# Performance work log

Hardware: AMD Instinct MI355X
Metric: run time of the kernel (lower is better)

## Reference

```python
import jax, jax.numpy as jnp
import numpy as np

N, NS, C, S = 262144, 8, 32, 8  # points, nsample, out_channels, share_channels
EPS = 1e-5

def _bn(x, g, b, axes):
    m = jnp.mean(x, axis=axes, keepdims=True)
    v = jnp.mean((x - m) ** 2, axis=axes, keepdims=True)
    return g * (x - m) * jax.lax.rsqrt(v + EPS) + b

def setup_inputs() -> dict:
    key = jax.random.key(0)
    ks = jax.random.split(key, 16)
    lin = lambda k, i, o: (jax.random.normal(k, (o, i), jnp.float32) / np.sqrt(i)).astype(jnp.float32)
    return {
        'p': jax.random.normal(ks[0], (N, 3), jnp.float32) * 10.0,
        'x': jax.random.normal(ks[1], (N, C), jnp.float32),
        'idx': jax.random.randint(ks[2], (N, NS), 0, N, jnp.int32),
        'Wq': lin(ks[3], C, C), 'bq': jnp.zeros((C,), jnp.float32),
        'Wk': lin(ks[4], C, C), 'bk': jnp.zeros((C,), jnp.float32),
        'Wv': lin(ks[5], C, C), 'bv': jnp.zeros((C,), jnp.float32),
        'Wp1': lin(ks[6], 3, 3), 'bp1': jnp.zeros((3,), jnp.float32),
        'gp': jnp.ones((3,), jnp.float32), 'bp': jnp.zeros((3,), jnp.float32),
        'Wp2': lin(ks[7], 3, C), 'bp2': jnp.zeros((C,), jnp.float32),
        'gw1': jnp.ones((C,), jnp.float32), 'bw1': jnp.zeros((C,), jnp.float32),
        'Ww1': lin(ks[8], C, C // S), 'bww1': jnp.zeros((C // S,), jnp.float32),
        'gw2': jnp.ones((C // S,), jnp.float32), 'bw2': jnp.zeros((C // S,), jnp.float32),
        'Ww2': lin(ks[9], C // S, C // S), 'bww2': jnp.zeros((C // S,), jnp.float32),
    }

def reference(p, x, idx, Wq, bq, Wk, bk, Wv, bv, Wp1, bp1, gp, bp, Wp2, bp2,
              gw1, bw1, Ww1, bww1, gw2, bw2, Ww2, bww2):
    n = x.shape[0]
    q = x @ Wq.T + bq                      # (n, C)
    k = x @ Wk.T + bk
    v = x @ Wv.T + bv
    # queryandgroup: gather neighbors, relative xyz (use_xyz=True for key path)
    p_r = p[idx] - p[:, None, :]           # (n, ns, 3)
    kg = k[idx]                            # (n, ns, C)
    vg = v[idx]                            # (n, ns, C)
    # linear_p: Linear(3,3) -> BN(3) (over n, ns) -> ReLU -> Linear(3, C)
    p_r = p_r @ Wp1.T + bp1
    p_r = jax.nn.relu(_bn(p_r, gp, bp, (0, 1)))
    p_r = p_r @ Wp2.T + bp2                # (n, ns, C)
    # out_channels // mid_channels == 1, so the .view(...).sum(2) is identity
    w = kg - q[:, None, :] + p_r           # (n, ns, C)
    # linear_w: BN(C) -> ReLU -> Linear(C, C//S) -> BN(C//S) -> ReLU -> Linear
    w = jax.nn.relu(_bn(w, gw1, bw1, (0, 1)))
    w = w @ Ww1.T + bww1                   # (n, ns, C//S)
    w = jax.nn.relu(_bn(w, gw2, bw2, (0, 1)))
    w = w @ Ww2.T + bww2
    w = jax.nn.softmax(w, axis=1)          # softmax over nsample
    # grouped weighted sum: (n, ns, S, C//S) * (n, ns, 1, C//S)
    out = ((vg + p_r).reshape(n, NS, S, C // S) * w[:, :, None, :]).sum(1)
    return out.reshape(n, C)
```

## Files before the change

kernel.cpp:

```cpp
#include <hip/hip_runtime.h>
#include <hip/hip_bf16.h>

#define NPTS   262144
#define NSAMP  8
#define NPAIR  (NPTS * NSAMP)
#define EPSV   1e-5f
#define INVCNT (1.0f / (float)NPAIR)
#define GSTAT  2048
#define PPB    (NPAIR / GSTAT)

typedef __hip_bfloat16 bf16;

template <typename T> __device__ __forceinline__ float cvt(T v);
template <> __device__ __forceinline__ float cvt<float>(float v) { return v; }
template <> __device__ __forceinline__ float cvt<bf16>(bf16 v) { return __bfloat162float(v); }

template <typename T> __device__ __forceinline__ T f2t(float v);
template <> __device__ __forceinline__ float f2t<float>(float v) { return v; }
template <> __device__ __forceinline__ bf16  f2t<bf16>(float v)  { return __float2bfloat16(v); }

__global__ void k_detect(const unsigned int* __restrict__ xw, int* __restrict__ flag)
{
    if (threadIdx.x == 0 && blockIdx.x == 0) {
        int cnt = 0;
        for (int i = 0; i < 256; ++i) {
            const unsigned int w = xw[i];
            const unsigned int e = (w >> 7) & 0xFF;
            if (e >= 110 && e <= 132) ++cnt;
        }
        flag[0] = (cnt >= 128) ? 0 : 1;
    }
}

template <typename T>
__global__ __launch_bounds__(256) void k_qkv(
    const T* __restrict__ x,
    const T* __restrict__ Wq, const T* __restrict__ bq,
    const T* __restrict__ Wk, const T* __restrict__ bk,
    const T* __restrict__ Wv, const T* __restrict__ bv,
    float* __restrict__ q, float* __restrict__ k, float* __restrict__ v,
    const int* __restrict__ flag, const int want)
{
    if (flag[0] != want) return;
    __shared__ float Wt[3][32][32];
    __shared__ float xs[8][32];
    const int t = threadIdx.x;
    for (int e = t; e < 1024; e += 256) {
        const int c = e >> 5, j = e & 31;
        Wt[0][j][c] = cvt<T>(Wq[e]);
        Wt[1][j][c] = cvt<T>(Wk[e]);
        Wt[2][j][c] = cvt<T>(Wv[e]);
    }
    __syncthreads();
    const int c = t & 31, pi = t >> 5;
    const float bqv = cvt<T>(bq[c]), bkv = cvt<T>(bk[c]), bvv = cvt<T>(bv[c]);
    const int base0 = blockIdx.x * 128;
    for (int it = 0; it < 16; ++it) {
        const int base = base0 + it * 8;
        __syncthreads();
        xs[t >> 5][t & 31] = cvt<T>(x[base * 32 + t]);
        __syncthreads();
        float aq = bqv, ak = bkv, av = bvv;
#pragma unroll
        for (int j = 0; j < 32; ++j) {
            const float xv = xs[pi][j];
            aq += Wt[0][j][c] * xv;
            ak += Wt[1][j][c] * xv;
            av += Wt[2][j][c] * xv;
        }
        const int o = (base + pi) * 32 + c;
        q[o] = aq; k[o] = ak; v[o] = av;
    }
}

template <typename T>
__global__ __launch_bounds__(256) void k_pr1(
    const T* __restrict__ p, const int* __restrict__ idx,
    const T* __restrict__ Wp1, const T* __restrict__ bp1,
    float* __restrict__ pr1, float* __restrict__ P1,
    const int* __restrict__ flag, const int want)
{
    if (flag[0] != want) return;
    float W[3][3], B[3];
#pragma unroll
    for (int a = 0; a < 3; ++a) {
        B[a] = cvt<T>(bp1[a]);
#pragma unroll
        for (int d = 0; d < 3; ++d) W[a][d] = cvt<T>(Wp1[a * 3 + d]);
    }
    const int t = threadIdx.x;
    const int base = blockIdx.x * PPB;
    float s[3] = {0.f, 0.f, 0.f}, ss[3] = {0.f, 0.f, 0.f};
    for (int it = 0; it < PPB; it += 256) {
        const int pid = base + it + t;
        const int i = pid >> 3;
        const int nj = idx[pid];
        const float d0 = cvt<T>(p[nj * 3 + 0]) - cvt<T>(p[i * 3 + 0]);
        const float d1 = cvt<T>(p[nj * 3 + 1]) - cvt<T>(p[i * 3 + 1]);
        const float d2 = cvt<T>(p[nj * 3 + 2]) - cvt<T>(p[i * 3 + 2]);
#pragma unroll
        for (int a = 0; a < 3; ++a) {
            const float r = W[a][0] * d0 + W[a][1] * d1 + W[a][2] * d2 + B[a];
            pr1[pid * 3 + a] = r;
            s[a] += r; ss[a] += r * r;
        }
    }
#pragma unroll
    for (int o = 32; o > 0; o >>= 1) {
#pragma unroll
        for (int a = 0; a < 3; ++a) { s[a] += __shfl_down(s[a], o); ss[a] += __shfl_down(ss[a], o); }
    }
    __shared__ float red[4][16];
    const int wid = t >> 6, lane = t & 63;
    if (lane == 0) {
#pragma unroll
        for (int u = 0; u < 16; ++u) red[wid][u] = 0.f;
#pragma unroll
        for (int a = 0; a < 3; ++a) { red[wid][a] = s[a]; red[wid][8 + a] = ss[a]; }
    }
    __syncthreads();
    if (t < 16) P1[blockIdx.x * 16 + t] = red[0][t] + red[1][t] + red[2][t] + red[3][t];
}

template <typename T, int NC_, int NP_>
__global__ __launch_bounds__(1024) void k_fin(
    const float* __restrict__ P, const int nblocks,
    const T* __restrict__ g, const T* __restrict__ b,
    float* __restrict__ A, float* __restrict__ Cc,
    const int* __restrict__ flag, const int want)
{
    if (flag[0] != want) return;
    constexpr int COLS = 2 * NP_;
    constexpr int GRP  = 1024 / COLS;
    const int t = threadIdx.x;
    const int c = t % COLS;
    const int gi = t / COLS;
    float acc = 0.f;
    for (int r = gi; r < nblocks; r += GRP) acc += P[r * COLS + c];
    __shared__ float red[1024];
    red[t] = acc;
    __syncthreads();
#pragma unroll
    for (int s = GRP >> 1; s > 0; s >>= 1) {
        if (gi < s) red[t] += red[t + s * COLS];
        __syncthreads();
    }
    if (t < NC_) {
        const float m = red[t] * INVCNT;
        const float var = red[NP_ + t] * INVCNT - m * m;
        const float a = cvt<T>(g[t]) * rsqrtf(var + EPSV);
        A[t] = a;
        Cc[t] = cvt<T>(b[t]) - a * m;
    }
}

template <typename T>
__global__ __launch_bounds__(256) void k_bn2stat(
    const int* __restrict__ idx, const float* __restrict__ pr1,
    const float* __restrict__ q, const float* __restrict__ k,
    const T* __restrict__ Wp2, const T* __restrict__ bp2,
    const float* __restrict__ coef, float* __restrict__ P2,
    const int* __restrict__ flag, const int want)
{
    if (flag[0] != want) return;
    const int t = threadIdx.x;
    const int c = t & 31;
    const int sub = t >> 5;
    const float a10 = coef[0], a11 = coef[1], a12 = coef[2];
    const float c10 = coef[8], c11 = coef[9], c12 = coef[10];
    const float w0 = cvt<T>(Wp2[c * 3 + 0]), w1 = cvt<T>(Wp2[c * 3 + 1]), w2 = cvt<T>(Wp2[c * 3 + 2]);
    const float bb = cvt<T>(bp2[c]);
    float s = 0.f, ss = 0.f;
    const int base = blockIdx.x * PPB;
    for (int it = 0; it < PPB; it += 32) {
        int pids[4], njs[4];
#pragma unroll
        for (int u = 0; u < 4; ++u) pids[u] = base + it + u * 8 + sub;
#pragma unroll
        for (int u = 0; u < 4; ++u) njs[u] = idx[pids[u]];
        float h[4][3];
#pragma unroll
        for (int u = 0; u < 4; ++u) {
            h[u][0] = fmaxf(a10 * pr1[pids[u] * 3 + 0] + c10, 0.f);
            h[u][1] = fmaxf(a11 * pr1[pids[u] * 3 + 1] + c11, 0.f);
            h[u][2] = fmaxf(a12 * pr1[pids[u] * 3 + 2] + c12, 0.f);
        }
        float kv[4], qv[4];
#pragma unroll
        for (int u = 0; u < 4; ++u) {
            kv[u] = k[(size_t)njs[u] * 32 + c];
            qv[u] = q[(size_t)(pids[u] >> 3) * 32 + c];
        }
#pragma unroll
        for (int u = 0; u < 4; ++u) {
            const float pr2 = w0 * h[u][0] + w1 * h[u][1] + w2 * h[u][2] + bb;
            const float wp = kv[u] - qv[u] + pr2;
            s += wp; ss += wp * wp;
        }
    }
    s += __shfl_down(s, 32); ss += __shfl_down(ss, 32);
    __shared__ float red[4][64];
    const int wid = t >> 6, lane = t & 63;
    if (lane < 32) { red[wid][lane] = s; red[wid][32 + lane] = ss; }
    __syncthreads();
    if (t < 64) P2[blockIdx.x * 64 + t] = red[0][t] + red[1][t] + red[2][t] + red[3][t];
}

template <typename T>
__global__ __launch_bounds__(256) void k_w1(
    const int* __restrict__ idx, const float* __restrict__ pr1,
    const float* __restrict__ q, const float* __restrict__ k,
    const T* __restrict__ Wp2, const T* __restrict__ bp2,
    const T* __restrict__ Ww1, const T* __restrict__ bww1,
    const float* __restrict__ coef, float* __restrict__ w1out, float* __restrict__ P3,
    const int* __restrict__ flag, const int want)
{
    if (flag[0] != want) return;
    __shared__ float sWp2[32][3], sbp2[32], sW1[4][32], sb1[4], sa2[32], sc2[32];
    const int t = threadIdx.x;
    if (t < 32) {
        sWp2[t][0] = cvt<T>(Wp2[t * 3 + 0]);
        sWp2[t][1] = cvt<T>(Wp2[t * 3 + 1]);
        sWp2[t][2] = cvt<T>(Wp2[t * 3 + 2]);
        sbp2[t] = cvt<T>(bp2[t]);
        sa2[t] = coef[16 + t];
        sc2[t] = coef[48 + t];
    }
    if (t < 4) sb1[t] = cvt<T>(bww1[t]);
    if (t < 128) sW1[t >> 5][t & 31] = cvt<T>(Ww1[t]);
    __syncthreads();
    const float a10 = coef[0], a11 = coef[1], a12 = coef[2];
    const float c10 = coef[8], c11 = coef[9], c12 = coef[10];
    float s[4] = {0.f, 0.f, 0.f, 0.f}, ss[4] = {0.f, 0.f, 0.f, 0.f};
    const int base = blockIdx.x * PPB;
    for (int it = 0; it < PPB; it += 256) {
        const int pid = base + it + t;
        const int i = pid >> 3;
        const int nj = idx[pid];
        const float h0 = fmaxf(a10 * pr1[pid * 3 + 0] + c10, 0.f);
        const float h1 = fmaxf(a11 * pr1[pid * 3 + 1] + c11, 0.f);
        const float h2 = fmaxf(a12 * pr1[pid * 3 + 2] + c12, 0.f);
        float acc[4] = {sb1[0], sb1[1], sb1[2], sb1[3]};
        const float* krow = k + (size_t)nj * 32;
        const float* qrow = q + (size_t)i * 32;
#pragma unroll
        for (int cc = 0; cc < 32; ++cc) {
            const float pr2 = sWp2[cc][0] * h0 + sWp2[cc][1] * h1 + sWp2[cc][2] * h2 + sbp2[cc];
            const float wp = krow[cc] - qrow[cc] + pr2;
            const float hh = fmaxf(sa2[cc] * wp + sc2[cc], 0.f);
            acc[0] += sW1[0][cc] * hh;
            acc[1] += sW1[1][cc] * hh;
            acc[2] += sW1[2][cc] * hh;
            acc[3] += sW1[3][cc] * hh;
        }
#pragma unroll
        for (int u = 0; u < 4; ++u) {
            w1out[pid * 4 + u] = acc[u];
            s[u] += acc[u]; ss[u] += acc[u] * acc[u];
        }
    }
#pragma unroll
    for (int o = 32; o > 0; o >>= 1) {
#pragma unroll
        for (int u = 0; u < 4; ++u) { s[u] += __shfl_down(s[u], o); ss[u] += __shfl_down(ss[u], o); }
    }
    __shared__ float red[4][8];
    const int wid = t >> 6, lane = t & 63;
    if (lane == 0) {
#pragma unroll
        for (int u = 0; u < 4; ++u) { red[wid][u] = s[u]; red[wid][4 + u] = ss[u]; }
    }
    __syncthreads();
    if (t < 8) P3[blockIdx.x * 8 + t] = red[0][t] + red[1][t] + red[2][t] + red[3][t];
}

template <typename T>
__global__ __launch_bounds__(256) void k_out(
    const int* __restrict__ idx, const float* __restrict__ pr1,
    const float* __restrict__ v, const float* __restrict__ w1in,
    const T* __restrict__ Wp2, const T* __restrict__ bp2,
    const T* __restrict__ Ww2, const T* __restrict__ bww2,
    const float* __restrict__ coef, T* __restrict__ out,
    const int* __restrict__ flag, const int want)
{
    if (flag[0] != want) return;
    const int t = threadIdx.x;
    const int c = t & 31, pi = t >> 5;
    const float a10 = coef[0], a11 = coef[1], a12 = coef[2];
    const float c10 = coef[8], c11 = coef[9], c12 = coef[10];
    const float wA = cvt<T>(Wp2[c * 3 + 0]), wB = cvt<T>(Wp2[c * 3 + 1]), wC = cvt<T>(Wp2[c * 3 + 2]);
    const float bb = cvt<T>(bp2[c]);
    const int tq = c & 3;
    float a3[4], c3[4], W2r[4];
#pragma unroll
    for (int u = 0; u < 4; ++u) {
        a3[u] = coef[80 + u]; c3[u] = coef[88 + u];
        W2r[u] = cvt<T>(Ww2[tq * 4 + u]);
    }
    const float b2r = cvt<T>(bww2[tq]);
    const int base0 = blockIdx.x * 128;
    for (int it = 0; it < 16; ++it) {
        const int i = base0 + it * 8 + pi;
        float lg[8];
#pragma unroll
        for (int j = 0; j < 8; ++j) {
            const float* wr = w1in + ((size_t)i * 8 + j) * 4;
            float l = b2r;
#pragma unroll
            for (int u = 0; u < 4; ++u) l += W2r[u] * fmaxf(a3[u] * wr[u] + c3[u], 0.f);
            lg[j] = l;
        }
        float m = lg[0];
#pragma unroll
        for (int j = 1; j < 8; ++j) m = fmaxf(m, lg[j]);
        float sum = 0.f;
#pragma unroll
        for (int j = 0; j < 8; ++j) { lg[j] = __expf(lg[j] - m); sum += lg[j]; }
        const float inv = 1.f / sum;
        float acc = 0.f;
#pragma unroll
        for (int j = 0; j < 8; ++j) {
            const int pid = i * 8 + j;
            const int nj = idx[pid];
            const float h0 = fmaxf(a10 * pr1[pid * 3 + 0] + c10, 0.f);
            const float h1 = fmaxf(a11 * pr1[pid * 3 + 1] + c11, 0.f);
            const float h2 = fmaxf(a12 * pr1[pid * 3 + 2] + c12, 0.f);
            const float pr2 = wA * h0 + wB * h1 + wC * h2 + bb;
            acc += (v[(size_t)nj * 32 + c] + pr2) * (lg[j] * inv);
        }
        out[(size_t)i * 32 + c] = f2t<T>(acc);
    }
}

template <typename T>
static void launch_pipeline(void* const* d_in, void* d_out, float* ws,
                            int* flag, const int want, hipStream_t stream)
{
    const T*   p    = (const T*)d_in[0];
    const T*   x    = (const T*)d_in[1];
    const int* idx  = (const int*)d_in[2];
    const T*   Wq   = (const T*)d_in[3];
    const T*   bq   = (const T*)d_in[4];
    const T*   Wk   = (const T*)d_in[5];
    const T*   bk   = (const T*)d_in[6];
    const T*   Wv   = (const T*)d_in[7];
    const T*   bv   = (const T*)d_in[8];
    const T*   Wp1  = (const T*)d_in[9];
    const T*   bp1  = (const T*)d_in[10];
    const T*   gp   = (const T*)d_in[11];
    const T*   bp   = (const T*)d_in[12];
    const T*   Wp2  = (const T*)d_in[13];
    const T*   bp2  = (const T*)d_in[14];
    const T*   gw1  = (const T*)d_in[15];
    const T*   bw1  = (const T*)d_in[16];
    const T*   Ww1  = (const T*)d_in[17];
    const T*   bww1 = (const T*)d_in[18];
    const T*   gw2  = (const T*)d_in[19];
    const T*   bw2  = (const T*)d_in[20];
    const T*   Ww2  = (const T*)d_in[21];
    const T*   bww2 = (const T*)d_in[22];
    T* out = (T*)d_out;

    float* coef = ws + 16;
    float* P1   = ws + 128;
    float* P2   = P1 + GSTAT * 16;
    float* P3   = P2 + GSTAT * 64;
    float* q    = ws + 262144;
    float* k    = q  + (size_t)NPTS * 32;
    float* v    = k  + (size_t)NPTS * 32;
    float* pr1  = v  + (size_t)NPTS * 32;
    float* w1   = pr1 + (size_t)NPAIR * 3;

    k_qkv<T><<<2048, 256, 0, stream>>>(x, Wq, bq, Wk, bk, Wv, bv, q, k, v, flag, want);
    k_pr1<T><<<GSTAT, 256, 0, stream>>>(p, idx, Wp1, bp1, pr1, P1, flag, want);
    k_fin<T, 3, 8><<<1, 1024, 0, stream>>>(P1, GSTAT, gp, bp, coef + 0, coef + 8, flag, want);
    k_bn2stat<T><<<GSTAT, 256, 0, stream>>>(idx, pr1, q, k, Wp2, bp2, coef, P2, flag, want);
    k_fin<T, 32, 32><<<1, 1024, 0, stream>>>(P2, GSTAT, gw1, bw1, coef + 16, coef + 48, flag, want);
    k_w1<T><<<GSTAT, 256, 0, stream>>>(idx, pr1, q, k, Wp2, bp2, Ww1, bww1, coef, w1, P3, flag, want);
    k_fin<T, 4, 4><<<1, 1024, 0, stream>>>(P3, GSTAT, gw2, bw2, coef + 80, coef + 88, flag, want);
    k_out<T><<<2048, 256, 0, stream>>>(idx, pr1, v, w1, Wp2, bp2, Ww2, bww2, coef, out, flag, want);
}

extern "C" void kernel_launch(void* const* d_in, const int* in_sizes, int n_in,
                              void* d_out, int out_size, void* d_ws, size_t ws_size,
                              hipStream_t stream)
{
    float* ws = (float*)d_ws;
    int* flag = (int*)ws;

    k_detect<<<1, 64, 0, stream>>>((const unsigned int*)d_in[1], flag);
    launch_pipeline<bf16>(d_in, d_out, ws, flag, 0, stream);
    launch_pipeline<float>(d_in, d_out, ws, flag, 1, stream);
}
```

Baseline: 525.1 us.

## Merge dtype-dispatched launches and vectorize gathers in w1 and out kernels

Collapses the two per-dtype pipelines, where half the launches exit early on a flag check, into a single set of kernels that branch on the flag internally. This halves the number of kernel launches. It also switches k_w1 to float4 loads of the gathered k and q rows, and makes k_out prefetch all neighbour indices, v values and pr1 terms before the softmax to expose memory-level parallelism. Adds launch_bounds occupancy hints and 64-bit indexing, at the cost of more registers from the prefetch arrays.

```diff
diff --git a/kernel.cpp b/kernel.cpp
--- a/kernel.cpp
+++ b/kernel.cpp
@@ -33,17 +33,14 @@
 }
 
 template <typename T>
-__global__ __launch_bounds__(256) void k_qkv(
+__device__ __forceinline__ void qkv_impl(
     const T* __restrict__ x,
     const T* __restrict__ Wq, const T* __restrict__ bq,
     const T* __restrict__ Wk, const T* __restrict__ bk,
     const T* __restrict__ Wv, const T* __restrict__ bv,
     float* __restrict__ q, float* __restrict__ k, float* __restrict__ v,
-    const int* __restrict__ flag, const int want)
-{
-    if (flag[0] != want) return;
-    __shared__ float Wt[3][32][32];
-    __shared__ float xs[8][32];
+    float (*Wt)[32][32], float (*xs)[32])
+{
     const int t = threadIdx.x;
     for (int e = t; e < 1024; e += 256) {
         const int c = e >> 5, j = e & 31;
@@ -58,7 +55,7 @@
     for (int it = 0; it < 16; ++it) {
         const int base = base0 + it * 8;
         __syncthreads();
-        xs[t >> 5][t & 31] = cvt<T>(x[base * 32 + t]);
+        xs[t >> 5][t & 31] = cvt<T>(x[(size_t)base * 32 + t]);
         __syncthreads();
         float aq = bqv, ak = bkv, av = bvv;
 #pragma unroll
@@ -68,19 +65,32 @@
             ak += Wt[1][j][c] * xv;
             av += Wt[2][j][c] * xv;
         }
-        const int o = (base + pi) * 32 + c;
+        const size_t o = (size_t)(base + pi) * 32 + c;
         q[o] = aq; k[o] = ak; v[o] = av;
     }
 }
 
+__global__ __launch_bounds__(256) void k_qkv(
+    const void* x, const void* Wq, const void* bq, const void* Wk, const void* bk,
+    const void* Wv, const void* bv,
+    float* q, float* k, float* v, const int* __restrict__ flag)
+{
+    __shared__ float Wt[3][32][32];
+    __shared__ float xs[8][32];
+    if (flag[0] == 0)
+        qkv_impl<bf16>((const bf16*)x, (const bf16*)Wq, (const bf16*)bq, (const bf16*)Wk,
+                       (const bf16*)bk, (const bf16*)Wv, (const bf16*)bv, q, k, v, Wt, xs);
+    else
+        qkv_impl<float>((const float*)x, (const float*)Wq, (const float*)bq, (const float*)Wk,
+                        (const float*)bk, (const float*)Wv, (const float*)bv, q, k, v, Wt, xs);
+}
+
 template <typename T>
-__global__ __launch_bounds__(256) void k_pr1(
+__device__ __forceinline__ void pr1_impl(
     const T* __restrict__ p, const int* __restrict__ idx,
     const T* __restrict__ Wp1, const T* __restrict__ bp1,
-    float* __restrict__ pr1, float* __restrict__ P1,
-    const int* __restrict__ flag, const int want)
-{
-    if (flag[0] != want) return;
+    float* __restrict__ pr1, float* __restrict__ P1, float (*red)[16])
+{
     float W[3][3], B[3];
 #pragma unroll
     for (int a = 0; a < 3; ++a) {
@@ -101,7 +111,7 @@
 #pragma unroll
         for (int a = 0; a < 3; ++a) {
             const float r = W[a][0] * d0 + W[a][1] * d1 + W[a][2] * d2 + B[a];
-            pr1[pid * 3 + a] = r;
+            pr1[(size_t)pid * 3 + a] = r;
             s[a] += r; ss[a] += r * r;
         }
     }
@@ -110,7 +120,6 @@
 #pragma unroll
         for (int a = 0; a < 3; ++a) { s[a] += __shfl_down(s[a], o); ss[a] += __shfl_down(ss[a], o); }
     }
-    __shared__ float red[4][16];
     const int wid = t >> 6, lane = t & 63;
     if (lane == 0) {
 #pragma unroll
@@ -122,14 +131,23 @@
     if (t < 16) P1[blockIdx.x * 16 + t] = red[0][t] + red[1][t] + red[2][t] + red[3][t];
 }
 
+__global__ __launch_bounds__(256) void k_pr1(
+    const void* p, const int* __restrict__ idx, const void* Wp1, const void* bp1,
+    float* pr1, float* P1, const int* __restrict__ flag)
+{
+    __shared__ float red[4][16];
+    if (flag[0] == 0)
+        pr1_impl<bf16>((const bf16*)p, idx, (const bf16*)Wp1, (const bf16*)bp1, pr1, P1, red);
+    else
+        pr1_impl<float>((const float*)p, idx, (const float*)Wp1, (const float*)bp1, pr1, P1, red);
+}
+
 template <typename T, int NC_, int NP_>
-__global__ __launch_bounds__(1024) void k_fin(
+__device__ __forceinline__ void fin_impl(
     const float* __restrict__ P, const int nblocks,
     const T* __restrict__ g, const T* __restrict__ b,
-    float* __restrict__ A, float* __restrict__ Cc,
-    const int* __restrict__ flag, const int want)
-{
-    if (flag[0] != want) return;
+    float* __restrict__ A, float* __restrict__ Cc, float* red)
+{
     constexpr int COLS = 2 * NP_;
     constexpr int GRP  = 1024 / COLS;
     const int t = threadIdx.x;
@@ -137,7 +155,6 @@
     const int gi = t / COLS;
     float acc = 0.f;
     for (int r = gi; r < nblocks; r += GRP) acc += P[r * COLS + c];
-    __shared__ float red[1024];
     red[t] = acc;
     __syncthreads();
 #pragma unroll
@@ -154,15 +171,25 @@
     }
 }
 
+template <int NC_, int NP_>
+__global__ __launch_bounds__(1024) void k_fin(
+    const float* P, const int nblocks, const void* g, const void* b,
+    float* A, float* Cc, const int* __restrict__ flag)
+{
+    __shared__ float red[1024];
+    if (flag[0] == 0)
+        fin_impl<bf16, NC_, NP_>(P, nblocks, (const bf16*)g, (const bf16*)b, A, Cc, red);
+    else
+        fin_impl<float, NC_, NP_>(P, nblocks, (const float*)g, (const float*)b, A, Cc, red);
+}
+
 template <typename T>
-__global__ __launch_bounds__(256) void k_bn2stat(
+__device__ __forceinline__ void bn2_impl(
     const int* __restrict__ idx, const float* __restrict__ pr1,
     const float* __restrict__ q, const float* __restrict__ k,
     const T* __restrict__ Wp2, const T* __restrict__ bp2,
-    const float* __restrict__ coef, float* __restrict__ P2,
-    const int* __restrict__ flag, const int want)
-{
-    if (flag[0] != want) return;
+    const float* __restrict__ coef, float* __restrict__ P2, float (*red)[64])
+{
     const int t = threadIdx.x;
     const int c = t & 31;
     const int sub = t >> 5;
@@ -181,9 +208,9 @@
         float h[4][3];
 #pragma unroll
         for (int u = 0; u < 4; ++u) {
-            h[u][0] = fmaxf(a10 * pr1[pids[u] * 3 + 0] + c10, 0.f);
-            h[u][1] = fmaxf(a11 * pr1[pids[u] * 3 + 1] + c11, 0.f);
-            h[u][2] = fmaxf(a12 * pr1[pids[u] * 3 + 2] + c12, 0.f);
+            h[u][0] = fmaxf(a10 * pr1[(size_t)pids[u] * 3 + 0] + c10, 0.f);
+            h[u][1] = fmaxf(a11 * pr1[(size_t)pids[u] * 3 + 1] + c11, 0.f);
+            h[u][2] = fmaxf(a12 * pr1[(size_t)pids[u] * 3 + 2] + c12, 0.f);
         }
         float kv[4], qv[4];
 #pragma unroll
@@ -199,35 +226,54 @@
         }
     }
     s += __shfl_down(s, 32); ss += __shfl_down(ss, 32);
-    __shared__ float red[4][64];
     const int wid = t >> 6, lane = t & 63;
     if (lane < 32) { red[wid][lane] = s; red[wid][32 + lane] = ss; }
     __syncthreads();
     if (t < 64) P2[blockIdx.x * 64 + t] = red[0][t] + red[1][t] + red[2][t] + red[3][t];
 }
 
+__global__ __launch_bounds__(256) void k_bn2stat(
+    const int* __restrict__ idx, const float* pr1, const float* q, const float* k,
+    const void* Wp2, const void* bp2, const float* coef, float* P2,
+    const int* __restrict__ flag)
+{
+    __shared__ float red[4][64];
+    if (flag[0] == 0)
+        bn2_impl<bf16>(idx, pr1, q, k, (const bf16*)Wp2, (const bf16*)bp2, coef, P2, red);
+    else
+        bn2_impl<float>(idx, pr1, q, k, (const float*)Wp2, (const float*)bp2, coef, P2, red);
+}
+
+struct ShW1 {
+    float Wp2c[32][3];
+    float bp2[32];
+    float W1[4][32];
+    float b1[4];
+    float a2[32];
+    float c2[32];
+    float red[4][8];
+};
+
 template <typename T>
-__global__ __launch_bounds__(256) void k_w1(
+__device__ __forceinline__ void w1_impl(
     const int* __restrict__ idx, const float* __restrict__ pr1,
     const float* __restrict__ q, const float* __restrict__ k,
     const T* __restrict__ Wp2, const T* __restrict__ bp2,
     const T* __restrict__ Ww1, const T* __restrict__ bww1,
     const float* __restrict__ coef, float* __restrict__ w1out, float* __restrict__ P3,
-    const int* __restrict__ flag, const int want)
-{
-    if (flag[0] != want) return;
-    __shared__ float sWp2[32][3], sbp2[32], sW1[4][32], sb1[4], sa2[32], sc2[32];
+    ShW1* sh)
+{
     const int t = threadIdx.x;
     if (t < 32) {
-        sWp2[t][0] = cvt<T>(Wp2[t * 3 + 0]);
-        sWp2[t][1] = cvt<T>(Wp2[t * 3 + 1]);
-        sWp2[t][2] = cvt<T>(Wp2[t * 3 + 2]);
-        sbp2[t] = cvt<T>(bp2[t]);
-        sa2[t] = coef[16 + t];
-        sc2[t] = coef[48 + t];
-    }
-    if (t < 4) sb1[t] = cvt<T>(bww1[t]);
-    if (t < 128) sW1[t >> 5][t & 31] = cvt<T>(Ww1[t]);
+        sh->Wp2c[t][0] = cvt<T>(Wp2[t * 3 + 0]);
+        sh->Wp2c[t][1] = cvt<T>(Wp2[t * 3 + 1]);
+        sh->Wp2c[t][2] = cvt<T>(Wp2[t * 3 + 2]);
+        sh->bp2[t] = cvt<T>(bp2[t]);
+        sh->a2[t] = coef[16 + t];
+        sh->c2[t] = coef[48 + t];
+    }
+    if (t < 4) sh->b1[t] = cvt<T>(bww1[t]);
+    if (t < 128) sh->W1[t >> 5][t & 31] = cvt<T>(Ww1[t]);
     __syncthreads();
     const float a10 = coef[0], a11 = coef[1], a12 = coef[2];
     const float c10 = coef[8], c11 = coef[9], c12 = coef[10];
@@ -237,53 +283,77 @@
         const int pid = base + it + t;
         const int i = pid >> 3;
         const int nj = idx[pid];
-        const float h0 = fmaxf(a10 * pr1[pid * 3 + 0] + c10, 0.f);
-        const float h1 = fmaxf(a11 * pr1[pid * 3 + 1] + c11, 0.f);
-        const float h2 = fmaxf(a12 * pr1[pid * 3 + 2] + c12, 0.f);
-        float acc[4] = {sb1[0], sb1[1], sb1[2], sb1[3]};
-        const float* krow = k + (size_t)nj * 32;
-        const float* qrow = q + (size_t)i * 32;
-#pragma unroll
-        for (int cc = 0; cc < 32; ++cc) {
-            const float pr2 = sWp2[cc][0] * h0 + sWp2[cc][1] * h1 + sWp2[cc][2] * h2 + sbp2[cc];
-            const float wp = krow[cc] - qrow[cc] + pr2;
-            const float hh = fmaxf(sa2[cc] * wp + sc2[cc], 0.f);
-            acc[0] += sW1[0][cc] * hh;
-            acc[1] += sW1[1][cc] * hh;
-            acc[2] += sW1[2][cc] * hh;
-            acc[3] += sW1[3][cc] * hh;
-        }
-#pragma unroll
-        for (int u = 0; u < 4; ++u) {
-            w1out[pid * 4 + u] = acc[u];
-            s[u] += acc[u]; ss[u] += acc[u] * acc[u];
-        }
+        const float4* k4 = (const float4*)(k + (size_t)nj * 32);
+        const float4* q4 = (const float4*)(q + (size_t)i * 32);
+        float4 kk[8], qq[8];
+#pragma unroll
+        for (int u = 0; u < 8; ++u) kk[u] = k4[u];
+#pragma unroll
+        for (int u = 0; u < 8; ++u) qq[u] = q4[u];
+        const float h0 = fmaxf(a10 * pr1[(size_t)pid * 3 + 0] + c10, 0.f);
+        const float h1 = fmaxf(a11 * pr1[(size_t)pid * 3 + 1] + c11, 0.f);
+        const float h2 = fmaxf(a12 * pr1[(size_t)pid * 3 + 2] + c12, 0.f);
+        float acc0 = sh->b1[0], acc1 = sh->b1[1], acc2 = sh->b1[2], acc3 = sh->b1[3];
+#pragma unroll
+        for (int u = 0; u < 8; ++u) {
+            const float kd[4] = {kk[u].x - qq[u].x, kk[u].y - qq[u].y,
+                                 kk[u].z - qq[u].z, kk[u].w - qq[u].w};
+#pragma unroll
+            for (int e = 0; e < 4; ++e) {
+                const int cc = u * 4 + e;
+                const float pr2 = sh->Wp2c[cc][0] * h0 + sh->Wp2c[cc][1] * h1
+                                + sh->Wp2c[cc][2] * h2 + sh->bp2[cc];
+                const float wp = kd[e] + pr2;
+                const float hh = fmaxf(sh->a2[cc] * wp + sh->c2[cc], 0.f);
+                acc0 += sh->W1[0][cc] * hh;
+                acc1 += sh->W1[1][cc] * hh;
+                acc2 += sh->W1[2][cc] * hh;
+                acc3 += sh->W1[3][cc] * hh;
+            }
+        }
+        float* wr = w1out + (size_t)pid * 4;
+        wr[0] = acc0; wr[1] = acc1; wr[2] = acc2; wr[3] = acc3;
+        s[0] += acc0; ss[0] += acc0 * acc0;
+        s[1] += acc1; ss[1] += acc1 * acc1;
+        s[2] += acc2; ss[2] += acc2 * acc2;
+        s[3] += acc3; ss[3] += acc3 * acc3;
     }
 #pragma unroll
     for (int o = 32; o > 0; o >>= 1) {
 #pragma unroll
         for (int u = 0; u < 4; ++u) { s[u] += __shfl_down(s[u], o); ss[u] += __shfl_down(ss[u], o); }
     }
-    __shared__ float red[4][8];
     const int wid = t >> 6, lane = t & 63;
     if (lane == 0) {
 #pragma unroll
-        for (int u = 0; u < 4; ++u) { red[wid][u] = s[u]; red[wid][4 + u] = ss[u]; }
-    }
-    __syncthreads();
-    if (t < 8) P3[blockIdx.x * 8 + t] = red[0][t] + red[1][t] + red[2][t] + red[3][t];
+        for (int u = 0; u < 4; ++u) { sh->red[wid][u] = s[u]; sh->red[wid][4 + u] = ss[u]; }
+    }
+    __syncthreads();
+    if (t < 8) P3[blockIdx.x * 8 + t] = sh->red[0][t] + sh->red[1][t] + sh->red[2][t] + sh->red[3][t];
+}
+
+__global__ __launch_bounds__(256, 4) void k_w1(
+    const int* __restrict__ idx, const float* pr1, const float* q, const float* k,
+    const void* Wp2, const void* bp2, const void* Ww1, const void* bww1,
+    const float* coef, float* w1out, float* P3, const int* __restrict__ flag)
+{
+    __shared__ ShW1 sh;
+    if (flag[0] == 0)
+        w1_impl<bf16>(idx, pr1, q, k, (const bf16*)Wp2, (const bf16*)bp2,
+                      (const bf16*)Ww1, (const bf16*)bww1, coef, w1out, P3, &sh);
+    else
+        w1_impl<float>(idx, pr1, q, k, (const float*)Wp2, (const float*)bp2,
+                       (const float*)Ww1, (const float*)bww1, coef, w1out, P3, &sh);
 }
 
 template <typename T>
-__global__ __launch_bounds__(256) void k_out(
+__device__ __forceinline__ void out_impl(
     const int* __restrict__ idx, const float* __restrict__ pr1,
     const float* __restrict__ v, const float* __restrict__ w1in,
     const T* __restrict__ Wp2, const T* __restrict__ bp2,
     const T* __restrict__ Ww2, const T* __restrict__ bww2,
-    const float* __restrict__ coef, T* __restrict__ out,
-    const int* __restrict__ flag, const int want)
-{
-    if (flag[0] != want) return;
+    const float* __restrict__ coef, T* __restrict__ out)
+{
     const int t = threadIdx.x;
     const int c = t & 31, pi = t >> 5;
     const float a10 = coef[0], a11 = coef[1], a12 = coef[2];
@@ -301,6 +371,12 @@
     const int base0 = blockIdx.x * 128;
     for (int it = 0; it < 16; ++it) {
         const int i = base0 + it * 8 + pi;
+        int njs[8];
+#pragma unroll
+        for (int j = 0; j < 8; ++j) njs[j] = idx[(size_t)i * 8 + j];
+        float vv[8];
+#pragma unroll
+        for (int j = 0; j < 8; ++j) vv[j] = v[(size_t)njs[j] * 32 + c];
         float lg[8];
 #pragma unroll
         for (int j = 0; j < 8; ++j) {
@@ -310,6 +386,14 @@
             for (int u = 0; u < 4; ++u) l += W2r[u] * fmaxf(a3[u] * wr[u] + c3[u], 0.f);
             lg[j] = l;
         }
+        float h[8][3];
+#pragma unroll
+        for (int j = 0; j < 8; ++j) {
+            const size_t pb = ((size_t)i * 8 + j) * 3;
+            h[j][0] = fmaxf(a10 * pr1[pb + 0] + c10, 0.f);
+            h[j][1] = fmaxf(a11 * pr1[pb + 1] + c11, 0.f);
+            h[j][2] = fmaxf(a12 * pr1[pb + 2] + c12, 0.f);
+        }
         float m = lg[0];
 #pragma unroll
         for (int j = 1; j < 8; ++j) m = fmaxf(m, lg[j]);
@@ -320,47 +404,56 @@
         float acc = 0.f;
 #pragma unroll
         for (int j = 0; j < 8; ++j) {
-            const int pid = i * 8 + j;
-            const int nj = idx[pid];
-            const float h0 = fmaxf(a10 * pr1[pid * 3 + 0] + c10, 0.f);
-            const float h1 = fmaxf(a11 * pr1[pid * 3 + 1] + c11, 0.f);
-            const float h2 = fmaxf(a12 * pr1[pid * 3 + 2] + c12, 0.f);
-            const float pr2 = wA * h0 + wB * h1 + wC * h2 + bb;
-            acc += (v[(size_t)nj * 32 + c] + pr2) * (lg[j] * inv);
+            const float pr2 = wA * h[j][0] + wB * h[j][1] + wC * h[j][2] + bb;
+            acc += (vv[j] + pr2) * (lg[j] * inv);
         }
         out[(size_t)i * 32 + c] = f2t<T>(acc);
     }
 }
 
-template <typename T>
-static void launch_pipeline(void* const* d_in, void* d_out, float* ws,
-                            int* flag, const int want, hipStream_t stream)
-{
-    const T*   p    = (const T*)d_in[0];
-    const T*   x    = (const T*)d_in[1];
-    const int* idx  = (const int*)d_in[2];
-    const T*   Wq   = (const T*)d_in[3];
-    const T*   bq   = (const T*)d_in[4];
-    const T*   Wk   = (const T*)d_in[5];
-    const T*   bk   = (const T*)d_in[6];
-    const T*   Wv   = (const T*)d_in[7];
-    const T*   bv   = (const T*)d_in[8];
-    const T*   Wp1  = (const T*)d_in[9];
-    const T*   bp1  = (const T*)d_in[10];
-    const T*   gp   = (const T*)d_in[11];
-    const T*   bp   = (const T*)d_in[12];
-    const T*   Wp2  = (const T*)d_in[13];
-    const T*   bp2  = (const T*)d_in[14];
-    const T*   gw1  = (const T*)d_in[15];
-    const T*   bw1  = (const T*)d_in[16];
-    const T*   Ww1  = (const T*)d_in[17];
-    const T*   bww1 = (const T*)d_in[18];
-    const T*   gw2  = (const T*)d_in[19];
-    const T*   bw2  = (const T*)d_in[20];
-    const T*   Ww2  = (const T*)d_in[21];
-    const T*   bww2 = (const T*)d_in[22];
-    T* out = (T*)d_out;
-
+__global__ __launch_bounds__(256, 4) void k_out(
+    const int* __restrict__ idx, const float* pr1, const float* v, const float* w1in,
+    const void* Wp2, const void* bp2, const void* Ww2, const void* bww2,
+    const float* coef, void* out, const int* __restrict__ flag)
+{
+    if (flag[0] == 0)
+        out_impl<bf16>(idx, pr1, v, w1in, (const bf16*)Wp2, (const bf16*)bp2,
+                       (const bf16*)Ww2, (const bf16*)bww2, coef, (bf16*)out);
+    else
+        out_impl<float>(idx, pr1, v, w1in, (const float*)Wp2, (const float*)bp2,
+                        (const float*)Ww2, (const float*)bww2, coef, (float*)out);
+}
+
+extern "C" void kernel_launch(void* const* d_in, const int* in_sizes, int n_in,
+                              void* d_out, int out_size, void* d_ws, size_t ws_size,
+                              hipStream_t stream)
+{
+    const void* p    = d_in[0];
+    const void* x    = d_in[1];
+    const int*  idx  = (const int*)d_in[2];
+    const void* Wq   = d_in[3];
+    const void* bq   = d_in[4];
+    const void* Wk   = d_in[5];
+    const void* bk   = d_in[6];
+    const void* Wv   = d_in[7];
+    const void* bv   = d_in[8];
+    const void* Wp1  = d_in[9];
+    const void* bp1  = d_in[10];
+    const void* gp   = d_in[11];
+    const void* bp   = d_in[12];
+    const void* Wp2  = d_in[13];
+    const void* bp2  = d_in[14];
+    const void* gw1  = d_in[15];
+    const void* bw1  = d_in[16];
+    const void* Ww1  = d_in[17];
+    const void* bww1 = d_in[18];
+    const void* gw2  = d_in[19];
+    const void* bw2  = d_in[20];
+    const void* Ww2  = d_in[21];
+    const void* bww2 = d_in[22];
+
+    float* ws = (float*)d_ws;
+    int* flag = (int*)ws;
     float* coef = ws + 16;
     float* P1   = ws + 128;
     float* P2   = P1 + GSTAT * 16;
@@ -371,24 +464,13 @@
     float* pr1  = v  + (size_t)NPTS * 32;
     float* w1   = pr1 + (size_t)NPAIR * 3;
 
-    k_qkv<T><<<2048, 256, 0, stream>>>(x, Wq, bq, Wk, bk, Wv, bv, q, k, v, flag, want);
-    k_pr1<T><<<GSTAT, 256, 0, stream>>>(p, idx, Wp1, bp1, pr1, P1, flag, want);
-    k_fin<T, 3, 8><<<1, 1024, 0, stream>>>(P1, GSTAT, gp, bp, coef + 0, coef + 8, flag, want);
-    k_bn2stat<T><<<GSTAT, 256, 0, stream>>>(idx, pr1, q, k, Wp2, bp2, coef, P2, flag, want);
-    k_fin<T, 32, 32><<<1, 1024, 0, stream>>>(P2, GSTAT, gw1, bw1, coef + 16, coef + 48, flag, want);
-    k_w1<T><<<GSTAT, 256, 0, stream>>>(idx, pr1, q, k, Wp2, bp2, Ww1, bww1, coef, w1, P3, flag, want);
-    k_fin<T, 4, 4><<<1, 1024, 0, stream>>>(P3, GSTAT, gw2, bw2, coef + 80, coef + 88, flag, want);
-    k_out<T><<<2048, 256, 0, stream>>>(idx, pr1, v, w1, Wp2, bp2, Ww2, bww2, coef, out, flag, want);
-}
-
-extern "C" void kernel_launch(void* const* d_in, const int* in_sizes, int n_in,
-                              void* d_out, int out_size, void* d_ws, size_t ws_size,
-                              hipStream_t stream)
-{
-    float* ws = (float*)d_ws;
-    int* flag = (int*)ws;
-
-    k_detect<<<1, 64, 0, stream>>>((const unsigned int*)d_in[1], flag);
-    launch_pipeline<bf16>(d_in, d_out, ws, flag, 0, stream);
-    launch_pipeline<float>(d_in, d_out, ws, flag, 1, stream);
-}
+    k_detect<<<1, 64, 0, stream>>>((const unsigned int*)x, flag);
+    k_qkv<<<2048, 256, 0, stream>>>(x, Wq, bq, Wk, bk, Wv, bv, q, k, v, flag);
+    k_pr1<<<GSTAT, 256, 0, stream>>>(p, idx, Wp1, bp1, pr1, P1, flag);
+    k_fin<3, 8><<<1, 1024, 0, stream>>>(P1, GSTAT, gp, bp, coef + 0, coef + 8, flag);
+    k_bn2stat<<<GSTAT, 256, 0, stream>>>(idx, pr1, q, k, Wp2, bp2, coef, P2, flag);
+    k_fin<32, 32><<<1, 1024, 0, stream>>>(P2, GSTAT, gw1, bw1, coef + 16, coef + 48, flag);
+    k_w1<<<GSTAT, 256, 0, stream>>>(idx, pr1, q, k, Wp2, bp2, Ww1, bww1, coef, w1, P3, flag);
+    k_fin<4, 4><<<1, 1024, 0, stream>>>(P3, GSTAT, gw2, bw2, coef + 80, coef + 88, flag);
+    k_out<<<2048, 256, 0, stream>>>(idx, pr1, v, w1, Wp2, bp2, Ww2, bww2, coef, d_out, flag);
+}
```

After: 1.223 ms. 2.33x slower.
